# Kernel tuning notes

Hardware: AMD Instinct MI355X
Metric: run time of the kernel (lower is better)

## Reference

```python
import jax, jax.numpy as jnp
import numpy as np

B, C, H, W = 4, 64, 64, 64  # x shape; mask is (B,1,8H,8W)


def _conv(x, w, pad=0):
    return jax.lax.conv_general_dilated(
        x, w, (1, 1), [(pad, pad), (pad, pad)],
        dimension_numbers=('NCHW', 'OIHW', 'NCHW'))


def _inorm(x, eps=1e-5):  # InstanceNorm2d, affine=False, biased var (torch default)
    mu = x.mean(axis=(2, 3), keepdims=True)
    var = x.var(axis=(2, 3), keepdims=True)
    return (x - mu) * jax.lax.rsqrt(var + eps)


def _forward(x, mask, kconv_w1, kconv_w2, fs_w1, fs_w2, fs_b2, fs_fuse_w):
    b, c, h, w = x.shape
    n = h * w
    # MaxPool2d(8,8) then binarize
    m = jax.lax.reduce_window(mask, -jnp.inf, jax.lax.max,
                              (1, 1, 8, 8), (1, 1, 8, 8), 'VALID')
    m = (m > 0).astype(x.dtype)
    back = 1.0 - m
    # ResidualBlock K_conv (shared for K and Q paths in original code)
    y = jax.nn.relu(_inorm(_conv(x, kconv_w1, pad=1)))
    y = _inorm(_conv(y, kconv_w2, pad=1))
    kx = jax.nn.relu(y + x)
    # L2-normalized K/Q over channel dim
    K = (kx * back).reshape(b, c, n)
    K = K / (jnp.linalg.norm(K, axis=1, keepdims=True) + 1e-8)
    Q = (kx * m).reshape(b, c, n)
    Q = Q / (jnp.linalg.norm(Q, axis=1, keepdims=True) + 1e-8)
    V = (x * back).reshape(b, c, n)
    # cosine-similarity score map, temperature 20
    score = jnp.einsum('bcq,bck->bqk', Q, K) * 20.0  # (b, n_q, n_k)
    qm = m.reshape(b, 1, n)      # query mask (foreground)
    km = back.reshape(b, 1, n)   # key mask (background)
    NEG = -1000000.0
    validx = score + (1.0 - km) * NEG + (1.0 - qm.transpose(0, 2, 1)) * NEG
    att = jax.nn.softmax(validx, axis=-1) * (qm.transpose(0, 2, 1) * km)
    # att_fore[b,c,q] = sum_k V[b,c,k] * att[b,q,k]
    att_fore = jnp.einsum('bck,bqk->bcq', V, att).reshape(b, c, h, w)
    # Fusion_score
    feat1 = _conv(jnp.concatenate([x * m, att_fore * m], axis=1), fs_w1)
    s = jax.nn.sigmoid(_conv(feat1, fs_w2) + fs_b2[None, :, None, None])
    fused = _conv(jnp.concatenate([x * m, att_fore * m * (1.0 - s)], axis=1), fs_fuse_w)
    fs_out = fused * m + x * (1.0 - m)
    out = fs_out * m + x * (1.0 - m)
    # visualization attention mask
    visatt = att.sum(axis=1).reshape(b, 1, h, w)
    attmask = jnp.repeat(jnp.repeat(visatt, 8, axis=2), 8, axis=3)  # nearest upsample x8
    attmask = attmask / attmask.max()
    return out, attmask


def setup_inputs() -> dict:
    key = jax.random.key(0)
    ks = jax.random.split(key, 8)

    def wgt(k, shape, fan_in):
        return jax.random.normal(k, shape, jnp.float32) / np.sqrt(fan_in)

    x = jax.random.normal(ks[0], (B, C, H, W), jnp.float32)
    # sparse foreground mask so maxpool(8x8)>0 yields a mixed fg/bg mask
    mask = (jax.random.uniform(ks[1], (B, 1, H * 8, W * 8)) < 0.01).astype(jnp.float32)
    return dict(
        x=x, mask=mask,
        kconv_w1=wgt(ks[2], (C, C, 3, 3), C * 9),
        kconv_w2=wgt(ks[3], (C, C, 3, 3), C * 9),
        fs_w1=wgt(ks[4], (C, 2 * C, 1, 1), 2 * C),
        fs_w2=wgt(ks[5], (C, C, 1, 1), C),
        fs_b2=jnp.zeros((C,), jnp.float32),
        fs_fuse_w=wgt(ks[6], (C, 2 * C, 1, 1), 2 * C),
    )


def reference(x, mask, kconv_w1, kconv_w2, fs_w1, fs_w2, fs_b2, fs_fuse_w):
    return _forward(x, mask, kconv_w1, kconv_w2, fs_w1, fs_w2, fs_b2, fs_fuse_w)
```

## Files before the change

### kernel.cpp

```cpp
#include <hip/hip_runtime.h>
#include <hip/hip_bf16.h>

typedef __hip_bfloat16 bf16;
typedef __attribute__((ext_vector_type(8))) short short8;
typedef __attribute__((ext_vector_type(4))) float f32x4;

#define BB 4
#define CC 64
#define NN 4096
#define MH 512
#define MW 512
#define LS 72

#define WB_AFC  ((size_t)0)
#define WB_DEN  ((size_t)4194304)
#define WB_VIS  ((size_t)4259840)
#define WB_QIX  ((size_t)4325376)
#define WB_KIX  ((size_t)4390912)
#define WB_MFL  ((size_t)4456448)
#define WB_CNT  ((size_t)4472832)
#define WB_STAT ((size_t)4472896)
#define WB_WT1  ((size_t)4476992)
#define WB_WT2  ((size_t)4550720)
#define WB_WFB  ((size_t)4624448)

__device__ __forceinline__ float b2f(bf16 v) { return __bfloat162float(v); }
__device__ __forceinline__ float us2f(unsigned short u) { return __uint_as_float(((unsigned)u) << 16); }
__device__ __forceinline__ unsigned short f2bu(float f) {
  bf16 h = __float2bfloat16(f);
  return *(unsigned short*)&h;
}

__global__ __launch_bounds__(256) void k_maxpool(const float* __restrict__ mask,
                                                 unsigned char* __restrict__ mfl,
                                                 float* __restrict__ vis,
                                                 float* __restrict__ gstat,
                                                 unsigned int* __restrict__ vmaxb) {
  int g = blockIdx.x * 256 + threadIdx.x;
  int o = g >> 2, sub = g & 3;
  int b = o >> 12, p = o & 4095;
  int py = p >> 6, px = p & 63;
  const float* mb = mask + (size_t)b * MH * MW + (py * 8 + sub * 2) * MW + px * 8;
  float mx = 0.f;
  #pragma unroll
  for (int dy = 0; dy < 2; ++dy) {
    const float4* r4 = (const float4*)(mb + dy * MW);
    float4 a = r4[0], c = r4[1];
    mx = fmaxf(mx, fmaxf(fmaxf(a.x, a.y), fmaxf(a.z, a.w)));
    mx = fmaxf(mx, fmaxf(fmaxf(c.x, c.y), fmaxf(c.z, c.w)));
  }
  mx = fmaxf(mx, __shfl_xor(mx, 1));
  mx = fmaxf(mx, __shfl_xor(mx, 2));
  if (sub == 0) {
    mfl[o] = (mx > 0.f) ? 1 : 0;
    vis[o] = 0.f;
  }
  if (g < 1024) gstat[g] = 0.f;
  if (g == 0) vmaxb[0] = 0u;
}

__global__ __launch_bounds__(64) void k_compact(const unsigned char* __restrict__ mfl,
                                                int* __restrict__ qidx, int* __restrict__ kidx,
                                                int* __restrict__ nq, int* __restrict__ nk) {
  int b = blockIdx.x, lane = threadIdx.x;
  int qb = 0, kb = 0;
  for (int it = 0; it < 64; ++it) {
    int p = it * 64 + lane;
    bool f = mfl[b * NN + p] != 0;
    unsigned long long bal = __ballot(f);
    int before = __popcll(bal & ((1ULL << lane) - 1ULL));
    if (f)  qidx[b * NN + qb + before] = p;
    if (!f) kidx[b * NN + kb + (lane - before)] = p;
    int cnt = __popcll(bal);
    qb += cnt; kb += 64 - cnt;
  }
  if (lane == 0) { nq[b] = qb; nk[b] = kb; }
}

__global__ __launch_bounds__(256) void k_xT(const float* __restrict__ x,
                                            unsigned short* __restrict__ xt) {
  int b = blockIdx.x >> 6, p0 = (blockIdx.x & 63) * 64;
  __shared__ float lx[64][65];
  int t = threadIdx.x;
  const float* xb = x + (size_t)b * CC * NN + p0;
  for (int idx = t; idx < 4096; idx += 256) {
    int c = idx >> 6, j = idx & 63;
    lx[j][c] = xb[c * NN + j];
  }
  __syncthreads();
  unsigned short* xo = xt + ((size_t)b * NN + p0) * 64;
  for (int idx = t; idx < 2048; idx += 256) {
    int j = idx >> 5, c2 = (idx & 31) * 2;
    ushort2 w2;
    w2.x = f2bu(lx[j][c2]);
    w2.y = f2bu(lx[j][c2 + 1]);
    *(ushort2*)&xo[j * 64 + c2] = w2;
  }
}

__global__ __launch_bounds__(256) void k_wprep(const float* __restrict__ w1,
                                               const float* __restrict__ w2,
                                               const float* __restrict__ fw1,
                                               const float* __restrict__ fw2,
                                               const float* __restrict__ fwf,
                                               unsigned short* __restrict__ wT1,
                                               unsigned short* __restrict__ wT2,
                                               unsigned short* __restrict__ wfb) {
  int i = blockIdx.x * 256 + threadIdx.x;
  if (i < 36864) {
    int tap = i >> 12;
    int rem = i & 4095;
    int co = rem >> 6, ci = rem & 63;
    int src = (co * 64 + ci) * 9 + tap;
    wT1[i] = f2bu(w1[src]);
    wT2[i] = f2bu(w2[src]);
  } else if (i < 57344) {
    int j = i - 36864;
    if (j < 8192)       wfb[j] = f2bu(fw1[j]);
    else if (j < 12288) wfb[j] = f2bu(fw2[j - 8192]);
    else                wfb[j] = f2bu(fwf[j - 12288]);
  }
}

template <bool NORM_IN>
__global__ __launch_bounds__(256) void k_convm(const unsigned short* __restrict__ src,
                                               const unsigned short* __restrict__ wT,
                                               const float* __restrict__ insum,
                                               const float* __restrict__ insq,
                                               unsigned short* __restrict__ dst,
                                               float* __restrict__ gsum,
                                               float* __restrict__ gsq) {
  int b = blockIdx.y;
  int r = blockIdx.x;
  __shared__ unsigned short bx[198 * LS];
  __shared__ float nmean[64], ninv[64];
  int t = threadIdx.x;
  if (NORM_IN) {
    if (t < 64) {
      float m = insum[b * 64 + t] * (1.f / NN);
      float v = fmaxf(insq[b * 64 + t] * (1.f / NN) - m * m, 0.f);
      nmean[t] = m; ninv[t] = rsqrtf(v + 1e-5f);
    }
    __syncthreads();
  }
  const unsigned short* sb = src + (size_t)b * NN * 64;
  for (int idx = t; idx < 198 * 8; idx += 256) {
    int row = idx >> 3, c8 = (idx & 7) * 8;
    int dy = row / 66;
    int cx = row - dy * 66 - 1;
    int rr = r + dy - 1;
    uint4 v = make_uint4(0u, 0u, 0u, 0u);
    if ((unsigned)rr < 64u && (unsigned)cx < 64u) {
      v = *(const uint4*)(sb + ((size_t)(rr * 64 + cx)) * 64 + c8);
      if (NORM_IN) {
        unsigned short* e = (unsigned short*)&v;
        #pragma unroll
        for (int j = 0; j < 8; ++j)
          e[j] = f2bu(fmaxf((us2f(e[j]) - nmean[c8 + j]) * ninv[c8 + j], 0.f));
      }
    }
    *(uint4*)&bx[row * LS + c8] = v;
  }
  __syncthreads();
  int lane = t & 63;
  int quad = lane >> 4, col = lane & 15;
  int qw = (t >> 6) * 16;
  f32x4 acc[4] = {{0.f,0.f,0.f,0.f},{0.f,0.f,0.f,0.f},{0.f,0.f,0.f,0.f},{0.f,0.f,0.f,0.f}};
  #pragma unroll
  for (int tap = 0; tap < 9; ++tap) {
    int dy = tap / 3, dx = tap - dy * 3 - 1;
    const unsigned short* wrow = wT + ((size_t)tap * 64 + qw + col) * 64;
    short8 a0 = *(const short8*)(wrow + quad * 8);
    short8 a1 = *(const short8*)(wrow + 32 + quad * 8);
    int rbase = dy * 66 + dx + 1;
    #pragma unroll
    for (int nt = 0; nt < 4; ++nt) {
      int row = rbase + nt * 16 + col;
      short8 b0 = *(const short8*)&bx[row * LS + quad * 8];
      short8 b1 = *(const short8*)&bx[row * LS + 32 + quad * 8];
      acc[nt] = __builtin_amdgcn_mfma_f32_16x16x32_bf16(a0, b0, acc[nt], 0, 0, 0);
      acc[nt] = __builtin_amdgcn_mfma_f32_16x16x32_bf16(a1, b1, acc[nt], 0, 0, 0);
    }
  }
  #pragma unroll
  for (int rr = 0; rr < 4; ++rr) {
    float s1 = acc[0][rr] + acc[1][rr] + acc[2][rr] + acc[3][rr];
    float s2 = acc[0][rr]*acc[0][rr] + acc[1][rr]*acc[1][rr]
             + acc[2][rr]*acc[2][rr] + acc[3][rr]*acc[3][rr];
    s1 += __shfl_xor(s1, 1); s2 += __shfl_xor(s2, 1);
    s1 += __shfl_xor(s1, 2); s2 += __shfl_xor(s2, 2);
    s1 += __shfl_xor(s1, 4); s2 += __shfl_xor(s2, 4);
    s1 += __shfl_xor(s1, 8); s2 += __shfl_xor(s2, 8);
    if (col == 0) {
      int co = qw + quad * 4 + rr;
      atomicAdd(&gsum[b * 64 + co], s1);
      atomicAdd(&gsq[b * 64 + co], s2);
    }
  }
  __syncthreads();
  #pragma unroll
  for (int nt = 0; nt < 4; ++nt)
    #pragma unroll
    for (int rr = 0; rr < 4; ++rr)
      bx[(nt * 16 + col) * LS + qw + quad * 4 + rr] = f2bu(acc[nt][rr]);
  __syncthreads();
  unsigned short* db = dst + ((size_t)b * NN + r * 64) * 64;
  for (int idx = t; idx < 512; idx += 256) {
    int px = idx >> 3, c8 = (idx & 7) * 8;
    *(uint4*)(db + (size_t)px * 64 + c8) = *(const uint4*)&bx[px * LS + c8];
  }
}

__global__ __launch_bounds__(256) void k_knorm(unsigned short* __restrict__ kxt,
                                               const unsigned short* __restrict__ xt,
                                               const float* __restrict__ gsum,
                                               const float* __restrict__ gsq,
                                               float* __restrict__ afc,
                                               float* __restrict__ den) {
  int b = blockIdx.x >> 6;
  int p0 = (blockIdx.x & 63) * 64;
  __shared__ float m2[64], i2[64];
  int t = threadIdx.x;
  if (t < 64) {
    float m = gsum[b * 64 + t] * (1.f / NN);
    float v = fmaxf(gsq[b * 64 + t] * (1.f / NN) - m * m, 0.f);
    m2[t] = m; i2[t] = rsqrtf(v + 1e-5f);
  }
  size_t gid = (size_t)blockIdx.x * 256 + t;
  float4 z4 = make_float4(0.f, 0.f, 0.f, 0.f);
  float4* az = (float4*)afc;
  #pragma unroll
  for (int j = 0; j < 4; ++j) az[gid + (size_t)j * 65536] = z4;
  if (gid < 16384) den[gid] = 0.f;
  __syncthreads();
  int px = t >> 2, c0 = (t & 3) * 16;
  size_t base = ((size_t)b * NN + p0 + px) * 64 + c0;
  unsigned short kv[16], xv[16];
  *(uint4*)&kv[0] = *(const uint4*)(kxt + base);
  *(uint4*)&kv[8] = *(const uint4*)(kxt + base + 8);
  *(uint4*)&xv[0] = *(const uint4*)(xt + base);
  *(uint4*)&xv[8] = *(const uint4*)(xt + base + 8);
  float v[16]; float ss = 0.f;
  #pragma unroll
  for (int j = 0; j < 16; ++j) {
    float f = fmaxf((us2f(kv[j]) - m2[c0 + j]) * i2[c0 + j] + us2f(xv[j]), 0.f);
    v[j] = f; ss += f * f;
  }
  ss += __shfl_xor(ss, 1);
  ss += __shfl_xor(ss, 2);
  float inv = 1.f / (sqrtf(ss) + 1e-8f);
  #pragma unroll
  for (int j = 0; j < 16; ++j) kv[j] = f2bu(v[j] * inv);
  *(uint4*)(kxt + base) = *(const uint4*)&kv[0];
  *(uint4*)(kxt + base + 8) = *(const uint4*)&kv[8];
}

__global__ __launch_bounds__(256) void k_att1(const unsigned short* __restrict__ khat,
                                              const unsigned short* __restrict__ xt,
                                              const int* __restrict__ qidx, const int* __restrict__ kidx,
                                              const int* __restrict__ nqv, const int* __restrict__ nkv,
                                              float* __restrict__ afc, float* __restrict__ den) {
  int b = blockIdx.y;
  int nqb = nqv[b], nkb = nkv[b];
  int q0 = (blockIdx.x >> 2) * 64;
  int part = blockIdx.x & 3;
  if (q0 >= nqb) return;
  int kbeg = (part * nkb) >> 2;
  int kend = ((part + 1) * nkb) >> 2;
  __shared__ unsigned short lq [64 * LS];
  __shared__ unsigned short lk [64 * LS];
  __shared__ unsigned short lvT[64 * LS];
  __shared__ unsigned short le [64 * LS];
  int t = threadIdx.x;
  int wave = t >> 6, lane = t & 63;
  int quad = lane >> 4, col = lane & 15;
  int qw = wave * 16;
  const int* qix = qidx + b * NN;
  const int* kix = kidx + b * NN;
  const unsigned short* khb = khat + (size_t)b * NN * 64;
  const unsigned short* xtb = xt + (size_t)b * NN * 64;
  for (int idx = t; idx < 512; idx += 256) {
    int q = idx >> 3, c8 = (idx & 7) * 8;
    uint4 v = make_uint4(0u, 0u, 0u, 0u);
    if (q0 + q < nqb) v = *(const uint4*)(khb + (size_t)qix[q0 + q] * 64 + c8);
    *(uint4*)&lq[q * LS + c8] = v;
  }
  f32x4 pv[4] = {{0.f,0.f,0.f,0.f},{0.f,0.f,0.f,0.f},{0.f,0.f,0.f,0.f},{0.f,0.f,0.f,0.f}};
  float dsum[4] = {0.f, 0.f, 0.f, 0.f};
  for (int j0 = kbeg; j0 < kend; j0 += 64) {
    __syncthreads();
    for (int idx = t; idx < 512; idx += 256) {
      int k = idx >> 3, c8 = (idx & 7) * 8;
      uint4 v = make_uint4(0u, 0u, 0u, 0u);
      uint4 vv = make_uint4(0u, 0u, 0u, 0u);
      if (j0 + k < kend) {
        int kp = kix[j0 + k];
        v  = *(const uint4*)(khb + (size_t)kp * 64 + c8);
        vv = *(const uint4*)(xtb + (size_t)kp * 64 + c8);
      }
      *(uint4*)&lk[k * LS + c8] = v;
      unsigned short* vs = (unsigned short*)&vv;
      #pragma unroll
      for (int jj = 0; jj < 8; ++jj) lvT[(c8 + jj) * LS + k] = vs[jj];
    }
    __syncthreads();
    #pragma unroll
    for (int kt = 0; kt < 4; ++kt) {
      f32x4 s = {0.f, 0.f, 0.f, 0.f};
      #pragma unroll
      for (int h = 0; h < 2; ++h) {
        short8 a  = *(const short8*)&lq[(qw + col) * LS + h * 32 + quad * 8];
        short8 bk = *(const short8*)&lk[(kt * 16 + col) * LS + h * 32 + quad * 8];
        s = __builtin_amdgcn_mfma_f32_16x16x32_bf16(a, bk, s, 0, 0, 0);
      }
      bool kval = (j0 + kt * 16 + col) < kend;
      #pragma unroll
      for (int r = 0; r < 4; ++r) {
        float e = kval ? __expf(20.f * s[r]) : 0.f;
        dsum[r] += e;
        le[(qw + quad * 4 + r) * LS + kt * 16 + col] = f2bu(e);
      }
    }
    __syncthreads();
    #pragma unroll
    for (int ct = 0; ct < 4; ++ct) {
      #pragma unroll
      for (int h = 0; h < 2; ++h) {
        short8 a  = *(const short8*)&le[(qw + col) * LS + h * 32 + quad * 8];
        short8 bv = *(const short8*)&lvT[(ct * 16 + col) * LS + h * 32 + quad * 8];
        pv[ct] = __builtin_amdgcn_mfma_f32_16x16x32_bf16(a, bv, pv[ct], 0, 0, 0);
      }
    }
  }
  #pragma unroll
  for (int r = 0; r < 4; ++r) {
    float v = dsum[r];
    v += __shfl_xor(v, 1); v += __shfl_xor(v, 2);
    v += __shfl_xor(v, 4); v += __shfl_xor(v, 8);
    dsum[r] = v;
  }
  #pragma unroll
  for (int r = 0; r < 4; ++r) {
    int qq = q0 + qw + quad * 4 + r;
    if (qq < nqb) {
      if (col == 0) atomicAdd(&den[b * NN + qq], dsum[r]);
      float* dst = afc + ((size_t)b * NN + qq) * 64;
      #pragma unroll
      for (int ct = 0; ct < 4; ++ct) atomicAdd(&dst[ct * 16 + col], pv[ct][r]);
    }
  }
}

__global__ __launch_bounds__(256) void k_att2(const unsigned short* __restrict__ khat,
                                              const int* __restrict__ qidx, const int* __restrict__ kidx,
                                              const int* __restrict__ nqv, const int* __restrict__ nkv,
                                              const float* __restrict__ den, float* __restrict__ vis) {
  int b = blockIdx.y;
  int nqb = nqv[b], nkb = nkv[b];
  int k0 = (blockIdx.x >> 2) * 64;
  int part = blockIdx.x & 3;
  if (k0 >= nkb) return;
  int qbeg = (part * nqb) >> 2;
  int qend = ((part + 1) * nqb) >> 2;
  __shared__ unsigned short lk[64 * LS];
  __shared__ unsigned short lq[64 * LS];
  __shared__ float w[64];
  int t = threadIdx.x;
  int wave = t >> 6, lane = t & 63;
  int quad = lane >> 4, col = lane & 15;
  int kw = wave * 16;
  const int* qix = qidx + b * NN;
  const int* kix = kidx + b * NN;
  const unsigned short* khb = khat + (size_t)b * NN * 64;
  for (int idx = t; idx < 512; idx += 256) {
    int k = idx >> 3, c8 = (idx & 7) * 8;
    uint4 v = make_uint4(0u, 0u, 0u, 0u);
    if (k0 + k < nkb) v = *(const uint4*)(khb + (size_t)kix[k0 + k] * 64 + c8);
    *(uint4*)&lk[k * LS + c8] = v;
  }
  float vacc[4] = {0.f, 0.f, 0.f, 0.f};
  for (int i0 = qbeg; i0 < qend; i0 += 64) {
    __syncthreads();
    for (int idx = t; idx < 512; idx += 256) {
      int q = idx >> 3, c8 = (idx & 7) * 8;
      uint4 v = make_uint4(0u, 0u, 0u, 0u);
      if (i0 + q < qend) v = *(const uint4*)(khb + (size_t)qix[i0 + q] * 64 + c8);
      *(uint4*)&lq[q * LS + c8] = v;
    }
    if (t < 64) {
      int qq = i0 + t;
      float d = (qq < qend) ? den[b * NN + qq] : 0.f;
      w[t] = (d > 0.f) ? 1.f / d : 0.f;
    }
    __syncthreads();
    #pragma unroll
    for (int qt = 0; qt < 4; ++qt) {
      f32x4 s = {0.f, 0.f, 0.f, 0.f};
      #pragma unroll
      for (int h = 0; h < 2; ++h) {
        short8 a  = *(const short8*)&lk[(kw + col) * LS + h * 32 + quad * 8];
        short8 bq = *(const short8*)&lq[(qt * 16 + col) * LS + h * 32 + quad * 8];
        s = __builtin_amdgcn_mfma_f32_16x16x32_bf16(a, bq, s, 0, 0, 0);
      }
      float wq = w[qt * 16 + col];
      #pragma unroll
      for (int r = 0; r < 4; ++r) vacc[r] += __expf(20.f * s[r]) * wq;
    }
  }
  #pragma unroll
  for (int r = 0; r < 4; ++r) {
    float v = vacc[r];
    v += __shfl_xor(v, 1); v += __shfl_xor(v, 2);
    v += __shfl_xor(v, 4); v += __shfl_xor(v, 8);
    int kk = k0 + kw + quad * 4 + r;
    if (col == 0 && kk < nkb) atomicAdd(&vis[b * NN + kix[kk]], v);
  }
}

__global__ __launch_bounds__(256) void k_copy(const uint4* __restrict__ src, uint4* __restrict__ dst, int n) {
  int i = blockIdx.x * 256 + threadIdx.x;
  if (i < n) dst[i] = src[i];
}

#define FS 136
__global__ __launch_bounds__(256) void k_fusionm(const unsigned short* __restrict__ xt,
                                                 const float* __restrict__ afc,
                                                 const float* __restrict__ den,
                                                 const int* __restrict__ qidx, const int* __restrict__ nqv,
                                                 const unsigned short* __restrict__ wall,
                                                 const float* __restrict__ b2,
                                                 float* __restrict__ outp) {
  int b = blockIdx.y;
  int nqb = nqv[b];
  int q0 = blockIdx.x * 64;
  if (q0 >= nqb) return;
  __shared__ unsigned short pxa[64 * FS];
  __shared__ unsigned short f1s[64 * LS];
  __shared__ int qpl[64];
  int t = threadIdx.x;
  int lane = t & 63;
  int quad = lane >> 4, col = lane & 15;
  int cb = (t >> 6) * 16;
  const int* qix = qidx + b * NN;
  const unsigned short* xtb = xt + (size_t)b * NN * 64;
  const unsigned short* w1b = wall;
  const unsigned short* w2b = wall + 8192;
  const unsigned short* wfb = wall + 12288;
  short8 a1[4], a2[2], af[4];
  #pragma unroll
  for (int kt = 0; kt < 4; ++kt) {
    a1[kt] = *(const short8*)&w1b[(cb + col) * 128 + kt * 32 + quad * 8];
    af[kt] = *(const short8*)&wfb[(cb + col) * 128 + kt * 32 + quad * 8];
  }
  #pragma unroll
  for (int kt = 0; kt < 2; ++kt)
    a2[kt] = *(const short8*)&w2b[(cb + col) * 64 + kt * 32 + quad * 8];
  float b2v[4];
  #pragma unroll
  for (int r = 0; r < 4; ++r) b2v[r] = b2[cb + quad * 4 + r];
  if (t < 64) qpl[t] = (q0 + t < nqb) ? qix[q0 + t] : -1;
  for (int idx = t; idx < 512; idx += 256) {
    int q = idx >> 3, c8 = (idx & 7) * 8;
    int qq = q0 + q;
    uint4 pv = make_uint4(0u, 0u, 0u, 0u);
    unsigned short pa8[8] = {0, 0, 0, 0, 0, 0, 0, 0};
    if (qq < nqb) {
      int qp = qix[qq];
      pv = *(const uint4*)(xtb + (size_t)qp * 64 + c8);
      float d = den[b * NN + qq];
      float invd = (d > 0.f) ? 1.f / d : 0.f;
      const float* ap = afc + ((size_t)b * NN + qq) * 64 + c8;
      #pragma unroll
      for (int j = 0; j < 8; ++j) pa8[j] = f2bu(ap[j] * invd);
    }
    *(uint4*)&pxa[q * FS + c8] = pv;
    *(uint4*)&pxa[q * FS + 64 + c8] = *(const uint4*)&pa8[0];
  }
  __syncthreads();
  #pragma unroll
  for (int qt = 0; qt < 4; ++qt) {
    f32x4 acc = {0.f, 0.f, 0.f, 0.f};
    #pragma unroll
    for (int kt = 0; kt < 4; ++kt) {
      short8 bfrag = *(const short8*)&pxa[(qt * 16 + col) * FS + kt * 32 + quad * 8];
      acc = __builtin_amdgcn_mfma_f32_16x16x32_bf16(a1[kt], bfrag, acc, 0, 0, 0);
    }
    #pragma unroll
    for (int r = 0; r < 4; ++r)
      f1s[(qt * 16 + col) * LS + cb + quad * 4 + r] = f2bu(acc[r]);
  }
  __syncthreads();
  #pragma unroll
  for (int qt = 0; qt < 4; ++qt) {
    f32x4 acc = {0.f, 0.f, 0.f, 0.f};
    #pragma unroll
    for (int kt = 0; kt < 2; ++kt) {
      short8 bfrag = *(const short8*)&f1s[(qt * 16 + col) * LS + kt * 32 + quad * 8];
      acc = __builtin_amdgcn_mfma_f32_16x16x32_bf16(a2[kt], bfrag, acc, 0, 0, 0);
    }
    #pragma unroll
    for (int r = 0; r < 4; ++r) {
      float sg = 1.f / (1.f + __expf(-(acc[r] + b2v[r])));
      int addr = (qt * 16 + col) * FS + 64 + cb + quad * 4 + r;
      pxa[addr] = f2bu(us2f(pxa[addr]) * (1.f - sg));
    }
  }
  __syncthreads();
  #pragma unroll
  for (int qt = 0; qt < 4; ++qt) {
    f32x4 acc = {0.f, 0.f, 0.f, 0.f};
    #pragma unroll
    for (int kt = 0; kt < 4; ++kt) {
      short8 bfrag = *(const short8*)&pxa[(qt * 16 + col) * FS + kt * 32 + quad * 8];
      acc = __builtin_amdgcn_mfma_f32_16x16x32_bf16(af[kt], bfrag, acc, 0, 0, 0);
    }
    int qp = qpl[qt * 16 + col];
    if (qp >= 0) {
      #pragma unroll
      for (int r = 0; r < 4; ++r)
        outp[((size_t)b * CC + cb + quad * 4 + r) * NN + qp] = acc[r];
    }
  }
}

__global__ __launch_bounds__(256) void k_vmax(const float* __restrict__ vis, unsigned int* __restrict__ vmaxb) {
  int i = blockIdx.x * 256 + threadIdx.x;
  float v = vis[i];
  #pragma unroll
  for (int off = 32; off > 0; off >>= 1) v = fmaxf(v, __shfl_down(v, off));
  if ((threadIdx.x & 63) == 0) atomicMax(vmaxb, __float_as_uint(v));
}

__global__ __launch_bounds__(256) void k_upsample(const float* __restrict__ vis,
                                                  const unsigned int* __restrict__ vmaxb,
                                                  float* __restrict__ out2) {
  int i = blockIdx.x * 256 + threadIdx.x;
  int b = i >> 18;
  int rem = i & 262143;
  int y = rem >> 9, x = rem & 511;
  float vm = __uint_as_float(vmaxb[0]);
  if (!(vm > 0.f)) vm = 1.f;
  out2[i] = vis[b * NN + (y >> 3) * 64 + (x >> 3)] / vm;
}

extern "C" void kernel_launch(void* const* d_in, const int* in_sizes, int n_in,
                              void* d_out, int out_size, void* d_ws, size_t ws_size,
                              hipStream_t stream) {
  const float* x    = (const float*)d_in[0];
  const float* mask = (const float*)d_in[1];
  const float* w1   = (const float*)d_in[2];
  const float* w2c  = (const float*)d_in[3];
  const float* fsw1 = (const float*)d_in[4];
  const float* fsw2 = (const float*)d_in[5];
  const float* fsb2 = (const float*)d_in[6];
  const float* fswf = (const float*)d_in[7];
  float* out = (float*)d_out;
  char* wsb = (char*)d_ws;

  float* afc = (float*)(wsb + WB_AFC);
  float* den = (float*)(wsb + WB_DEN);
  float* vis = (float*)(wsb + WB_VIS);
  int* qidx  = (int*)(wsb + WB_QIX);
  int* kidx  = (int*)(wsb + WB_KIX);
  unsigned char* mfl = (unsigned char*)(wsb + WB_MFL);
  int* nq = (int*)(wsb + WB_CNT);
  int* nk = nq + 4;
  unsigned int* vmaxb = (unsigned int*)(nq + 8);
  float* gstat = (float*)(wsb + WB_STAT);
  float* gsum1 = gstat;
  float* gsq1  = gstat + 256;
  float* gsum2 = gstat + 512;
  float* gsq2  = gstat + 768;
  unsigned short* wT1 = (unsigned short*)(wsb + WB_WT1);
  unsigned short* wT2 = (unsigned short*)(wsb + WB_WT2);
  unsigned short* wall = (unsigned short*)(wsb + WB_WFB);
  unsigned short* y1t = (unsigned short*)(wsb + WB_AFC);

  unsigned short* kxt = (unsigned short*)out;
  unsigned short* khat = kxt;
  unsigned short* xt = (unsigned short*)(out + 1048576);

  k_maxpool<<<256, 256, 0, stream>>>(mask, mfl, vis, gstat, vmaxb);
  k_compact<<<4, 64, 0, stream>>>(mfl, qidx, kidx, nq, nk);
  k_xT<<<256, 256, 0, stream>>>(x, xt);
  k_wprep<<<224, 256, 0, stream>>>(w1, w2c, fsw1, fsw2, fswf, wT1, wT2, wall);
  k_convm<false><<<dim3(64, BB), 256, 0, stream>>>(xt, wT1, nullptr, nullptr, y1t, gsum1, gsq1);
  k_convm<true><<<dim3(64, BB), 256, 0, stream>>>(y1t, wT2, gsum1, gsq1, kxt, gsum2, gsq2);
  k_knorm<<<256, 256, 0, stream>>>(kxt, xt, gsum2, gsq2, afc, den);
  k_att1<<<dim3(256, BB), 256, 0, stream>>>(khat, xt, qidx, kidx, nq, nk, afc, den);
  k_att2<<<dim3(256, BB), 256, 0, stream>>>(khat, qidx, kidx, nq, nk, den, vis);
  k_copy<<<1024, 256, 0, stream>>>((const uint4*)x, (uint4*)out, 262144);
  k_fusionm<<<dim3(64, BB), 256, 0, stream>>>(xt, afc, den, qidx, nq, wall, fsb2, out);
  k_vmax<<<64, 256, 0, stream>>>(vis, vmaxb);
  k_upsample<<<4096, 256, 0, stream>>>(vis, vmaxb, out + 1048576);
}
```

Measured before the change: 196.9 us.

## Switch attention kernels to 32x32x16 MFMA tiles with swizzled V transpose

Both attention kernels now use 32x32x16 bf16 MFMA instead of 16x16x32, with waves tiled 2x2 over the 64x64 query/key block. This gives more work per instruction and fewer LDS fragment reads. The V tile transpose into LDS now packs two keys per 32-bit store and uses an XOR swizzle to cut bank conflicts and store count. The trade-offs are heavier register use (16-float accumulators) and more shuffle steps in the reductions.

```diff
diff --git a/kernel.cpp b/kernel.cpp
--- a/kernel.cpp
+++ b/kernel.cpp
@@ -4,6 +4,7 @@
 typedef __hip_bfloat16 bf16;
 typedef __attribute__((ext_vector_type(8))) short short8;
 typedef __attribute__((ext_vector_type(4))) float f32x4;
+typedef __attribute__((ext_vector_type(16))) float f32x16;
 
 #define BB 4
 #define CC 64
@@ -273,8 +274,8 @@
   __shared__ unsigned short le [64 * LS];
   int t = threadIdx.x;
   int wave = t >> 6, lane = t & 63;
-  int quad = lane >> 4, col = lane & 15;
-  int qw = wave * 16;
+  int l31 = lane & 31, lhi = lane >> 5;
+  int qh = wave >> 1, kh = wave & 1;
   const int* qix = qidx + b * NN;
   const int* kix = kidx + b * NN;
   const unsigned short* khb = khat + (size_t)b * NN * 64;
@@ -285,69 +286,78 @@
     if (q0 + q < nqb) v = *(const uint4*)(khb + (size_t)qix[q0 + q] * 64 + c8);
     *(uint4*)&lq[q * LS + c8] = v;
   }
-  f32x4 pv[4] = {{0.f,0.f,0.f,0.f},{0.f,0.f,0.f,0.f},{0.f,0.f,0.f,0.f},{0.f,0.f,0.f,0.f}};
-  float dsum[4] = {0.f, 0.f, 0.f, 0.f};
+  f32x16 pv, dsum;
+  #pragma unroll
+  for (int i = 0; i < 16; ++i) { pv[i] = 0.f; dsum[i] = 0.f; }
+  int kp2 = t >> 3, vc8 = (t & 7) * 8, vcc = (t & 7);
   for (int j0 = kbeg; j0 < kend; j0 += 64) {
     __syncthreads();
     for (int idx = t; idx < 512; idx += 256) {
       int k = idx >> 3, c8 = (idx & 7) * 8;
       uint4 v = make_uint4(0u, 0u, 0u, 0u);
-      uint4 vv = make_uint4(0u, 0u, 0u, 0u);
-      if (j0 + k < kend) {
-        int kp = kix[j0 + k];
-        v  = *(const uint4*)(khb + (size_t)kp * 64 + c8);
-        vv = *(const uint4*)(xtb + (size_t)kp * 64 + c8);
+      if (j0 + k < kend) v = *(const uint4*)(khb + (size_t)kix[j0 + k] * 64 + c8);
+      *(uint4*)&lk[k * LS + c8] = v;
+    }
+    {
+      uint4 v0 = make_uint4(0u, 0u, 0u, 0u);
+      uint4 v1 = make_uint4(0u, 0u, 0u, 0u);
+      int ka = j0 + 2 * kp2, kb2 = ka + 1;
+      if (ka  < kend) v0 = *(const uint4*)(xtb + (size_t)kix[ka]  * 64 + vc8);
+      if (kb2 < kend) v1 = *(const uint4*)(xtb + (size_t)kix[kb2] * 64 + vc8);
+      const unsigned short* e0 = (const unsigned short*)&v0;
+      const unsigned short* e1 = (const unsigned short*)&v1;
+      int pbase = kp2 & 3, prun = kp2 >> 2;
+      int pp = pbase + (((prun) ^ vcc) << 2);
+      #pragma unroll
+      for (int jj = 0; jj < 8; ++jj) {
+        int c = vc8 + jj;
+        unsigned int w2 = (unsigned)e0[jj] | ((unsigned)e1[jj] << 16);
+        *(unsigned int*)&lvT[c * LS + pp * 2] = w2;
       }
-      *(uint4*)&lk[k * LS + c8] = v;
-      unsigned short* vs = (unsigned short*)&vv;
-      #pragma unroll
-      for (int jj = 0; jj < 8; ++jj) lvT[(c8 + jj) * LS + k] = vs[jj];
     }
     __syncthreads();
-    #pragma unroll
-    for (int kt = 0; kt < 4; ++kt) {
-      f32x4 s = {0.f, 0.f, 0.f, 0.f};
-      #pragma unroll
-      for (int h = 0; h < 2; ++h) {
-        short8 a  = *(const short8*)&lq[(qw + col) * LS + h * 32 + quad * 8];
-        short8 bk = *(const short8*)&lk[(kt * 16 + col) * LS + h * 32 + quad * 8];
-        s = __builtin_amdgcn_mfma_f32_16x16x32_bf16(a, bk, s, 0, 0, 0);
-      }
-      bool kval = (j0 + kt * 16 + col) < kend;
-      #pragma unroll
-      for (int r = 0; r < 4; ++r) {
-        float e = kval ? __expf(20.f * s[r]) : 0.f;
-        dsum[r] += e;
-        le[(qw + quad * 4 + r) * LS + kt * 16 + col] = f2bu(e);
-      }
+    f32x16 s;
+    #pragma unroll
+    for (int i = 0; i < 16; ++i) s[i] = 0.f;
+    #pragma unroll
+    for (int ks = 0; ks < 4; ++ks) {
+      short8 a  = *(const short8*)&lq[(qh * 32 + l31) * LS + ks * 16 + lhi * 8];
+      short8 bk = *(const short8*)&lk[(kh * 32 + l31) * LS + ks * 16 + lhi * 8];
+      s = __builtin_amdgcn_mfma_f32_32x32x16_bf16(a, bk, s, 0, 0, 0);
+    }
+    bool kval = (j0 + kh * 32 + l31) < kend;
+    #pragma unroll
+    for (int reg = 0; reg < 16; ++reg) {
+      float e = kval ? __expf(20.f * s[reg]) : 0.f;
+      dsum[reg] += e;
+      int row = (reg & 3) + 8 * (reg >> 2) + 4 * lhi;
+      le[(qh * 32 + row) * LS + kh * 32 + l31] = f2bu(e);
     }
     __syncthreads();
-    #pragma unroll
-    for (int ct = 0; ct < 4; ++ct) {
-      #pragma unroll
-      for (int h = 0; h < 2; ++h) {
-        short8 a  = *(const short8*)&le[(qw + col) * LS + h * 32 + quad * 8];
-        short8 bv = *(const short8*)&lvT[(ct * 16 + col) * LS + h * 32 + quad * 8];
-        pv[ct] = __builtin_amdgcn_mfma_f32_16x16x32_bf16(a, bv, pv[ct], 0, 0, 0);
-      }
-    }
-  }
-  #pragma unroll
-  for (int r = 0; r < 4; ++r) {
-    float v = dsum[r];
-    v += __shfl_xor(v, 1); v += __shfl_xor(v, 2);
-    v += __shfl_xor(v, 4); v += __shfl_xor(v, 8);
-    dsum[r] = v;
-  }
-  #pragma unroll
-  for (int r = 0; r < 4; ++r) {
-    int qq = q0 + qw + quad * 4 + r;
-    if (qq < nqb) {
-      if (col == 0) atomicAdd(&den[b * NN + qq], dsum[r]);
-      float* dst = afc + ((size_t)b * NN + qq) * 64;
-      #pragma unroll
-      for (int ct = 0; ct < 4; ++ct) atomicAdd(&dst[ct * 16 + col], pv[ct][r]);
-    }
+    int c = kh * 32 + l31;
+    int c37 = (c >> 3) & 7;
+    #pragma unroll
+    for (int ks = 0; ks < 4; ++ks) {
+      short8 a  = *(const short8*)&le[(qh * 32 + l31) * LS + ks * 16 + lhi * 8];
+      int run = ks * 2 + lhi;
+      short8 bv = *(const short8*)&lvT[c * LS + ((run ^ c37) << 3)];
+      pv = __builtin_amdgcn_mfma_f32_32x32x16_bf16(a, bv, pv, 0, 0, 0);
+    }
+  }
+  #pragma unroll
+  for (int reg = 0; reg < 16; ++reg) {
+    float v = dsum[reg];
+    v += __shfl_xor(v, 1); v += __shfl_xor(v, 2); v += __shfl_xor(v, 4);
+    v += __shfl_xor(v, 8); v += __shfl_xor(v, 16);
+    int row = (reg & 3) + 8 * (reg >> 2) + 4 * lhi;
+    int qq = q0 + qh * 32 + row;
+    if (l31 == 0 && qq < nqb) atomicAdd(&den[b * NN + qq], v);
+  }
+  #pragma unroll
+  for (int reg = 0; reg < 16; ++reg) {
+    int row = (reg & 3) + 8 * (reg >> 2) + 4 * lhi;
+    int qq = q0 + qh * 32 + row;
+    if (qq < nqb) atomicAdd(&afc[((size_t)b * NN + qq) * 64 + kh * 32 + l31], pv[reg]);
   }
 }
 
@@ -367,8 +377,8 @@
   __shared__ float w[64];
   int t = threadIdx.x;
   int wave = t >> 6, lane = t & 63;
-  int quad = lane >> 4, col = lane & 15;
-  int kw = wave * 16;
+  int l31 = lane & 31, lhi = lane >> 5;
+  int kh = wave >> 1, qh = wave & 1;
   const int* qix = qidx + b * NN;
   const int* kix = kidx + b * NN;
   const unsigned short* khb = khat + (size_t)b * NN * 64;
@@ -378,7 +388,9 @@
     if (k0 + k < nkb) v = *(const uint4*)(khb + (size_t)kix[k0 + k] * 64 + c8);
     *(uint4*)&lk[k * LS + c8] = v;
   }
-  float vacc[4] = {0.f, 0.f, 0.f, 0.f};
+  f32x16 vacc;
+  #pragma unroll
+  for (int i = 0; i < 16; ++i) vacc[i] = 0.f;
   for (int i0 = qbeg; i0 < qend; i0 += 64) {
     __syncthreads();
     for (int idx = t; idx < 512; idx += 256) {
@@ -393,27 +405,27 @@
       w[t] = (d > 0.f) ? 1.f / d : 0.f;
     }
     __syncthreads();
-    #pragma unroll
-    for (int qt = 0; qt < 4; ++qt) {
-      f32x4 s = {0.f, 0.f, 0.f, 0.f};
-      #pragma unroll
-      for (int h = 0; h < 2; ++h) {
-        short8 a  = *(const short8*)&lk[(kw + col) * LS + h * 32 + quad * 8];
-        short8 bq = *(const short8*)&lq[(qt * 16 + col) * LS + h * 32 + quad * 8];
-        s = __builtin_amdgcn_mfma_f32_16x16x32_bf16(a, bq, s, 0, 0, 0);
-      }
-      float wq = w[qt * 16 + col];
-      #pragma unroll
-      for (int r = 0; r < 4; ++r) vacc[r] += __expf(20.f * s[r]) * wq;
-    }
-  }
-  #pragma unroll
-  for (int r = 0; r < 4; ++r) {
-    float v = vacc[r];
-    v += __shfl_xor(v, 1); v += __shfl_xor(v, 2);
-    v += __shfl_xor(v, 4); v += __shfl_xor(v, 8);
-    int kk = k0 + kw + quad * 4 + r;
-    if (col == 0 && kk < nkb) atomicAdd(&vis[b * NN + kix[kk]], v);
+    f32x16 s;
+    #pragma unroll
+    for (int i = 0; i < 16; ++i) s[i] = 0.f;
+    #pragma unroll
+    for (int ks = 0; ks < 4; ++ks) {
+      short8 a  = *(const short8*)&lk[(kh * 32 + l31) * LS + ks * 16 + lhi * 8];
+      short8 bq = *(const short8*)&lq[(qh * 32 + l31) * LS + ks * 16 + lhi * 8];
+      s = __builtin_amdgcn_mfma_f32_32x32x16_bf16(a, bq, s, 0, 0, 0);
+    }
+    float wq = w[qh * 32 + l31];
+    #pragma unroll
+    for (int reg = 0; reg < 16; ++reg) vacc[reg] += __expf(20.f * s[reg]) * wq;
+  }
+  #pragma unroll
+  for (int reg = 0; reg < 16; ++reg) {
+    float v = vacc[reg];
+    v += __shfl_xor(v, 1); v += __shfl_xor(v, 2); v += __shfl_xor(v, 4);
+    v += __shfl_xor(v, 8); v += __shfl_xor(v, 16);
+    int row = (reg & 3) + 8 * (reg >> 2) + 4 * lhi;
+    int kk = k0 + kh * 32 + row;
+    if (l31 == 0 && kk < nkb) atomicAdd(&vis[b * NN + kix[kk]], v);
   }
 }
 
```

After: 200.6 us. About the same (+1.9%).
